# Optimization experiments

Hardware: AMD Instinct MI355X
Metric: run time of the kernel (lower is better)

## Reference

```python
import jax, jax.numpy as jnp
import numpy as np

L1_COST = 1000.0
ENTROPY_COST = 5e-05


def setup_inputs() -> dict:
    key = jax.random.key(0)
    k1, k2 = jax.random.split(key)
    inputs = jax.random.normal(k1, (8, 4096, 256), dtype=jnp.float32)
    # xavier_uniform for [K, D]: bound = sqrt(6/(K+D))
    K, D = 1024, 256
    bound = np.sqrt(6.0 / (K + D)).astype(np.float32)
    codebook = jax.random.uniform(k2, (K, D), dtype=jnp.float32, minval=-bound, maxval=bound)
    return {"inputs": inputs, "codebook": codebook}


def reference(inputs, codebook):
    D = codebook.shape[1]
    flat = inputs.reshape(-1, D)                                  # [N, D]
    norm_C = codebook / jnp.linalg.norm(codebook, axis=1, keepdims=True)   # [K, D]
    flat = flat / jnp.linalg.norm(flat, axis=1, keepdims=True)    # [N, D]
    distances = jax.nn.softmax(flat @ norm_C.T, axis=1)           # [N, K]
    reconstruction = (distances @ norm_C).reshape(inputs.shape)   # [B, S, D]
    # l1_loss(distances, zeros) == mean(|distances|)
    l1 = jnp.mean(jnp.abs(distances))
    # entropy term: mean_i sum_k [ -log_softmax(distances) @ distances.T ]_{ik}
    # = mean_i ( -log_softmax(distances)_i . colsum(distances) ), an O(N*K) equivalent
    log_sm = jax.nn.log_softmax(distances, axis=1)                # [N, K]
    col_sum = jnp.sum(distances, axis=0)                          # [K]
    entropy = jnp.mean(-(log_sm @ col_sum))
    loss = L1_COST * l1 + ENTROPY_COST * entropy
    return reconstruction, loss
```

## Files before the change

### kernel.cpp

```cpp
#include <hip/hip_runtime.h>
#include <cstdint>

#define N_ROWS 32768
#define KDIM 1024
#define DDIM 256

typedef __attribute__((ext_vector_type(8))) short bf16x8;
typedef __attribute__((ext_vector_type(4))) float f32x4;

__device__ __forceinline__ unsigned short f2bf(float f) {
  unsigned int u = __float_as_uint(f);
  u += 0x7FFFu + ((u >> 16) & 1u);
  return (unsigned short)(u >> 16);
}

__device__ __forceinline__ void gload_lds16(const void* g, void* l) {
  __builtin_amdgcn_global_load_lds(
      (const __attribute__((address_space(1))) unsigned int*)(uintptr_t)g,
      (__attribute__((address_space(3))) unsigned int*)(unsigned int)(uintptr_t)l,
      16, 0, 0);
}


__global__ __launch_bounds__(256) void k_norm_cb(const float* __restrict__ cb,
                                                 unsigned short* __restrict__ Cn,
                                                 unsigned short* __restrict__ CnT) {
  const int wid = threadIdx.x >> 6, lane = threadIdx.x & 63;
  const int k = blockIdx.x * 4 + wid;
  float4 v = ((const float4*)(cb + (size_t)k * DDIM))[lane];
  float s = v.x * v.x + v.y * v.y + v.z * v.z + v.w * v.w;
#pragma unroll
  for (int m = 32; m; m >>= 1) s += __shfl_xor(s, m, 64);
  const float rn = 1.0f / sqrtf(s);
  ushort4 p;
  p.x = f2bf(v.x * rn); p.y = f2bf(v.y * rn);
  p.z = f2bf(v.z * rn); p.w = f2bf(v.w * rn);
  const int kb = lane >> 3;
  const int physA = ((lane & 7) >> 1) ^ (k & 3);
  *(ushort4*)(Cn + (size_t)(k >> 6) * 16384 + kb * 2048 + (k & 63) * 32 + physA * 8 + (lane & 1) * 4) = p;
  const int sgl = k >> 5, c31 = k & 31, ch = c31 >> 3, cw = c31 & 7;
  const unsigned short pv[4] = {p.x, p.y, p.z, p.w};
#pragma unroll
  for (int j = 0; j < 4; ++j) {
    const int d = lane * 4 + j;
    CnT[(size_t)sgl * 8192 + d * 32 + ((ch ^ j) * 8) + cw] = pv[j];
  }
}

__global__ __launch_bounds__(512, 2) void k_all(const float* __restrict__ x,
                                                const unsigned short* __restrict__ Cn,
                                                const unsigned short* __restrict__ CnT,
                                                float* __restrict__ part,
                                                float* __restrict__ lse_part,
                                                float* __restrict__ out) {
  __shared__ unsigned short Cb[4][16384];
  __shared__ unsigned short Ps[128 * 72];
  __shared__ float csl[1024];
  __shared__ float rs[128], qs[128], irl[128];
  __shared__ float lse_sh[2];

  const int tid = threadIdx.x, wid = tid >> 6, lane = tid & 63;
  const int l15 = lane & 15, l4 = lane >> 4;
  const int wm = wid >> 1, wn = wid & 1;
  const int rb = blockIdx.x;
  if (tid < 128) { rs[tid] = 0.f; qs[tid] = 0.f; }
  for (int j = tid; j < 1024; j += 512) csl[j] = 0.f;

#pragma unroll
  for (int i = 0; i < 4; ++i) {
    const int off = i * 8192 + wid * 1024 + lane * 16;
    gload_lds16((const char*)Cn + off, (char*)Cb[2] + off);
    gload_lds16((const char*)Cn + 32768 + off, (char*)Cb[3] + off);
  }

  unsigned short* Xs = &Cb[0][0];
#pragma unroll
  for (int p16 = 0; p16 < 16; ++p16) {
    const int row = p16 * 8 + wid;
    float4 v = ((const float4*)(x + (size_t)(rb * 128 + row) * DDIM))[lane];
    float s = v.x * v.x + v.y * v.y + v.z * v.z + v.w * v.w;
#pragma unroll
    for (int m = 32; m; m >>= 1) s += __shfl_xor(s, m, 64);
    const float rn = 1.0f / sqrtf(s);
    ushort4 p;
    p.x = f2bf(v.x * rn); p.y = f2bf(v.y * rn);
    p.z = f2bf(v.z * rn); p.w = f2bf(v.w * rn);
    *(ushort4*)&Xs[(lane >> 3) * 4096 + row * 32 + (lane & 7) * 4] = p;
  }
  __syncthreads();
  bf16x8 areg[2][8];
#pragma unroll
  for (int mi = 0; mi < 2; ++mi)
#pragma unroll
    for (int kb = 0; kb < 8; ++kb)
      areg[mi][kb] = *(const bf16x8*)&Xs[kb * 4096 + (wm * 32 + mi * 16 + l15) * 32 + l4 * 8];

  const int xsw = l4 ^ (l15 & 3);

  float se[2][4], sq[2][4];
#pragma unroll
  for (int mi = 0; mi < 2; ++mi)
#pragma unroll
    for (int reg = 0; reg < 4; ++reg) { se[mi][reg] = 0.f; sq[mi][reg] = 0.f; }
  for (int kt = 0; kt < 16; ++kt) {
    __syncthreads();
    {
      const char* src = (kt <= 13) ? (const char*)Cn + (size_t)(kt + 2) * 32768
                      : (kt == 14) ? (const char*)Cn
                                   : (const char*)CnT;
      char* dst = (char*)Cb[kt & 3];
#pragma unroll
      for (int i = 0; i < 4; ++i) {
        const int off = i * 8192 + wid * 1024 + lane * 16;
        gload_lds16(src + off, dst + off);
      }
    }
    const unsigned short* B = Cb[(kt + 2) & 3];
    f32x4 acc[2][2] = {};
#pragma unroll
    for (int kb = 0; kb < 8; ++kb) {
      bf16x8 b[2];
#pragma unroll
      for (int ni = 0; ni < 2; ++ni)
        b[ni] = *(const bf16x8*)&B[kb * 2048 + (wn * 32 + ni * 16 + l15) * 32 + xsw * 8];
#pragma unroll
      for (int mi = 0; mi < 2; ++mi)
#pragma unroll
        for (int ni = 0; ni < 2; ++ni)
          acc[mi][ni] = __builtin_amdgcn_mfma_f32_16x16x32_bf16(areg[mi][kb], b[ni], acc[mi][ni], 0, 0, 0);
    }
#pragma unroll
    for (int mi = 0; mi < 2; ++mi)
#pragma unroll
      for (int reg = 0; reg < 4; ++reg)
#pragma unroll
        for (int ni = 0; ni < 2; ++ni) {
          const float e = __expf(acc[mi][ni][reg]);
          se[mi][reg] += e; sq[mi][reg] += e * e;
        }
  }
#pragma unroll
  for (int mi = 0; mi < 2; ++mi)
#pragma unroll
    for (int reg = 0; reg < 4; ++reg) {
#pragma unroll
      for (int m = 1; m < 16; m <<= 1) {
        se[mi][reg] += __shfl_xor(se[mi][reg], m, 64);
        sq[mi][reg] += __shfl_xor(sq[mi][reg], m, 64);
      }
    }
  if (l15 == 0) {
#pragma unroll
    for (int mi = 0; mi < 2; ++mi)
#pragma unroll
      for (int reg = 0; reg < 4; ++reg) {
        const int row = wm * 32 + mi * 16 + l4 * 4 + reg;
        atomicAdd(&rs[row], se[mi][reg]);
        atomicAdd(&qs[row], sq[mi][reg]);
      }
  }
  __syncthreads();
  if (tid < 128) {
    const float r = rs[tid];
    const float ir = 1.0f / r;
    irl[tid] = ir;
    float lse = logf((float)(KDIM + 1) + 0.5f * qs[tid] * ir * ir);
#pragma unroll
    for (int m = 32; m; m >>= 1) lse += __shfl_xor(lse, m, 64);
    if ((tid & 63) == 0) lse_sh[tid >> 6] = lse;
  }
  __syncthreads();
  float ir[2][4];
#pragma unroll
  for (int mi = 0; mi < 2; ++mi)
#pragma unroll
    for (int reg = 0; reg < 4; ++reg)
      ir[mi][reg] = irl[wm * 32 + mi * 16 + l4 * 4 + reg];

  f32x4 O[2][8] = {};
  const int psw_r = l15 >> 1;
  for (int kt = 0; kt < 16; ++kt) {
    const int cslot = (kt & 1) ? 0 : 2;
    const int tslot = cslot | 1;
    const int nslot = (kt & 1) ? 2 : 0;
    if (kt < 15) {
#pragma unroll
      for (int i = 0; i < 4; ++i) {
        const int off = i * 8192 + wid * 1024 + lane * 16;
        gload_lds16((const char*)Cn + (size_t)(kt + 1) * 32768 + off, (char*)Cb[nslot] + off);
      }
    }
    f32x4 S[2][2] = {};
#pragma unroll
    for (int kb = 0; kb < 8; ++kb) {
      bf16x8 b[2];
#pragma unroll
      for (int ni = 0; ni < 2; ++ni)
        b[ni] = *(const bf16x8*)&Cb[cslot][kb * 2048 + (wn * 32 + ni * 16 + l15) * 32 + xsw * 8];
#pragma unroll
      for (int mi = 0; mi < 2; ++mi)
#pragma unroll
        for (int ni = 0; ni < 2; ++ni)
          S[mi][ni] = __builtin_amdgcn_mfma_f32_16x16x32_bf16(areg[mi][kb], b[ni], S[mi][ni], 0, 0, 0);
    }
    float cs[2] = {0.f, 0.f};
#pragma unroll
    for (int mi = 0; mi < 2; ++mi)
#pragma unroll
      for (int reg = 0; reg < 4; ++reg) {
        const int row = wm * 32 + mi * 16 + l4 * 4 + reg;
        const int pswz = (l4 * 2 + (reg >> 1)) & 7;
#pragma unroll
        for (int ni = 0; ni < 2; ++ni) {
          const float e = __expf(S[mi][ni][reg]);
          const int chl = wn * 4 + ni * 2 + (l15 >> 3);
          Ps[row * 72 + ((chl ^ pswz) * 8) + (l15 & 7)] = f2bf(e);
          cs[ni] += e * ir[mi][reg];
        }
      }
#pragma unroll
    for (int ni = 0; ni < 2; ++ni) {
      float v = cs[ni];
      v += __shfl_xor(v, 16, 64);
      v += __shfl_xor(v, 32, 64);
      if (lane < 16) atomicAdd(&csl[kt * 64 + wn * 32 + ni * 16 + l15], v);
    }
    __syncthreads();
    if (kt < 15) {
#pragma unroll
      for (int i = 0; i < 4; ++i) {
        const int off = i * 8192 + wid * 1024 + lane * 16;
        gload_lds16((const char*)CnT + (size_t)(kt + 1) * 32768 + off, (char*)Cb[nslot + 1] + off);
      }
    }
#pragma unroll
    for (int kb2 = 0; kb2 < 2; ++kb2) {
      bf16x8 a2[2], b2[8];
#pragma unroll
      for (int mi = 0; mi < 2; ++mi) {
        const int row = wm * 32 + mi * 16 + l15;
        a2[mi] = *(const bf16x8*)&Ps[row * 72 + (((kb2 * 4 + l4) ^ psw_r) * 8)];
      }
#pragma unroll
      for (int ni = 0; ni < 8; ++ni) {
        const int d = wn * 128 + ni * 16 + l15;
        b2[ni] = *(const bf16x8*)&Cb[tslot][kb2 * 8192 + d * 32 + xsw * 8];
      }
#pragma unroll
      for (int mi = 0; mi < 2; ++mi)
#pragma unroll
        for (int ni = 0; ni < 8; ++ni)
          O[mi][ni] = __builtin_amdgcn_mfma_f32_16x16x32_bf16(a2[mi], b2[ni], O[mi][ni], 0, 0, 0);
    }
    __syncthreads();
  }

#pragma unroll
  for (int mi = 0; mi < 2; ++mi)
#pragma unroll
    for (int reg = 0; reg < 4; ++reg) {
      const int row = wm * 32 + mi * 16 + l4 * 4 + reg;
      const float irv = ir[mi][reg];
#pragma unroll
      for (int ni = 0; ni < 8; ++ni) {
        const int d = wn * 128 + ni * 16 + l15;
        out[(size_t)(rb * 128 + row) * DDIM + d] = O[mi][ni][reg] * irv;
      }
    }
  for (int j = tid; j < 1024; j += 512) part[rb * 1024 + j] = csl[j];
  if (tid == 0) lse_part[rb] = lse_sh[0] + lse_sh[1];
}

__global__ __launch_bounds__(256) void k_final(const float* __restrict__ part,
                                               const float* __restrict__ lse_part,
                                               float* __restrict__ acc3) {
  __shared__ float sh1[4], sh2[4], shl[4];
  const int tid = threadIdx.x, lane = tid & 63, w = tid >> 6;
  const int bh = tid & 15;
  const int kh = tid >> 4;
  const int k = blockIdx.x * 16 + kh;
  float s = 0.f;
#pragma unroll
  for (int m = 0; m < 16; ++m) s += part[(size_t)(bh * 16 + m) * 1024 + k];
#pragma unroll
  for (int m = 1; m < 16; m <<= 1) s += __shfl_xor(s, m, 64);
  float s1 = ((lane & 15) == 0) ? s : 0.f;
  float s2 = ((lane & 15) == 0) ? s * s : 0.f;
  s1 += __shfl_xor(s1, 16, 64); s2 += __shfl_xor(s2, 16, 64);
  s1 += __shfl_xor(s1, 32, 64); s2 += __shfl_xor(s2, 32, 64);
  if (lane == 0) { sh1[w] = s1; sh2[w] = s2; }
  float l = 0.f;
  if (blockIdx.x == 0) {
    l = lse_part[tid];
#pragma unroll
    for (int m = 1; m < 64; m <<= 1) l += __shfl_xor(l, m, 64);
  }
  if (lane == 0) shl[w] = l;
  __syncthreads();
  if (tid == 0) {
    atomicAdd(&acc3[0], sh1[0] + sh1[1] + sh1[2] + sh1[3]);
    atomicAdd(&acc3[1], sh2[0] + sh2[1] + sh2[2] + sh2[3]);
    if (blockIdx.x == 0) atomicAdd(&acc3[2], shl[0] + shl[1] + shl[2] + shl[3]);
  }
}

__global__ __launch_bounds__(64) void k_loss(const float* __restrict__ acc3,
                                             float* __restrict__ out) {
  if (threadIdx.x == 0) {
    const double S = acc3[0];
    const double Q = acc3[1];
    const double L = acc3[2];
    const double entropy = (S * L - Q) / (double)N_ROWS;
    const double l1 = S / ((double)N_ROWS * (double)KDIM);
    out[(size_t)N_ROWS * DDIM] = (float)(1000.0 * l1 + 5e-5 * entropy);
  }
}

extern "C" void kernel_launch(void* const* d_in, const int* in_sizes, int n_in,
                              void* d_out, int out_size, void* d_ws, size_t ws_size,
                              hipStream_t stream) {
  const float* x = (const float*)d_in[0];
  const float* cb = (const float*)d_in[1];
  float* out = (float*)d_out;
  char* ws = (char*)d_ws;

  unsigned short* Cn  = (unsigned short*)(ws + 0);
  unsigned short* CnT = (unsigned short*)(ws + 524288);
  float* part         = (float*)(ws + 1048576);
  float* lse_part     = (float*)(ws + 2097152);
  float* acc3         = (float*)(ws + 2098176);

  hipMemsetAsync(acc3, 0, 16, stream);
  k_norm_cb<<<256, 256, 0, stream>>>(cb, Cn, CnT);
  k_all<<<256, 512, 0, stream>>>(x, Cn, CnT, part, lse_part, out);
  k_final<<<64, 256, 0, stream>>>(part, lse_part, acc3);
  k_loss<<<1, 64, 0, stream>>>(acc3, out);
}
```

Baseline: 152.3 us.

## Halve row tile to 64, shrink LDS ring, use global atomics for reductions

The fused kernel now processes 64 rows per block instead of 128, across 512 blocks. It uses a smaller 64KB double-buffered LDS ring and splits the second pass into 32 half-width codebook tiles, which lets more blocks be resident per CU. Column sums and log-sum-exp partials are accumulated with global atomics, replacing the separate per-block partial buffers and the extra final reduction kernel. In exchange, each block re-streams the full codebook twice, so total codebook traffic doubles, and float atomic accumulation order becomes nondeterministic.

Result: slower. 174.6 us (+14.6%).

```diff
diff --git a/kernel.cpp b/kernel.cpp
--- a/kernel.cpp
+++ b/kernel.cpp
@@ -21,6 +21,23 @@
       16, 0, 0);
 }
 
+
+__device__ __forceinline__ void stage_cn32(const unsigned short* Cn, char* dstBase, int kt, int tid) {
+  const int t = kt >> 1, h = kt & 1;
+#pragma unroll
+  for (int i = 0; i < 2; ++i) {
+    const int o = i * 4096 + tid * 8;
+    const size_t g = (size_t)t * 16384 + (size_t)(o >> 10) * 2048 + (size_t)h * 1024 + (o & 1023);
+    gload_lds16((const char*)(Cn + g), dstBase + (size_t)o * 2);
+  }
+}
+__device__ __forceinline__ void stage_cnt32(const unsigned short* CnT, char* dstBase, int kt, int tid) {
+#pragma unroll
+  for (int i = 0; i < 2; ++i) {
+    const int o = i * 4096 + tid * 8;
+    gload_lds16((const char*)(CnT + (size_t)kt * 8192 + o), dstBase + (size_t)o * 2);
+  }
+}
 
 __global__ __launch_bounds__(256) void k_norm_cb(const float* __restrict__ cb,
                                                  unsigned short* __restrict__ Cn,
@@ -47,37 +64,35 @@
   }
 }
 
-__global__ __launch_bounds__(512, 2) void k_all(const float* __restrict__ x,
+__global__ __launch_bounds__(512, 4) void k_all(const float* __restrict__ x,
                                                 const unsigned short* __restrict__ Cn,
                                                 const unsigned short* __restrict__ CnT,
-                                                float* __restrict__ part,
-                                                float* __restrict__ lse_part,
+                                                float* __restrict__ colsum_g,
+                                                float* __restrict__ accL,
                                                 float* __restrict__ out) {
-  __shared__ unsigned short Cb[4][16384];
-  __shared__ unsigned short Ps[128 * 72];
+  __shared__ __align__(16) unsigned short Ring[32768];
+  __shared__ __align__(16) unsigned short Ps[64 * 40];
   __shared__ float csl[1024];
-  __shared__ float rs[128], qs[128], irl[128];
-  __shared__ float lse_sh[2];
+  __shared__ float rs[64], qs[64], irl[64];
 
   const int tid = threadIdx.x, wid = tid >> 6, lane = tid & 63;
   const int l15 = lane & 15, l4 = lane >> 4;
   const int wm = wid >> 1, wn = wid & 1;
   const int rb = blockIdx.x;
-  if (tid < 128) { rs[tid] = 0.f; qs[tid] = 0.f; }
+  if (tid < 64) { rs[tid] = 0.f; qs[tid] = 0.f; }
   for (int j = tid; j < 1024; j += 512) csl[j] = 0.f;
 
 #pragma unroll
   for (int i = 0; i < 4; ++i) {
-    const int off = i * 8192 + wid * 1024 + lane * 16;
-    gload_lds16((const char*)Cn + off, (char*)Cb[2] + off);
-    gload_lds16((const char*)Cn + 32768 + off, (char*)Cb[3] + off);
-  }
-
-  unsigned short* Xs = &Cb[0][0];
-#pragma unroll
-  for (int p16 = 0; p16 < 16; ++p16) {
-    const int row = p16 * 8 + wid;
-    float4 v = ((const float4*)(x + (size_t)(rb * 128 + row) * DDIM))[lane];
+    const int off = i * 8192 + tid * 16;
+    gload_lds16((const char*)Cn + off, (char*)Ring + off);
+  }
+
+  unsigned short* Xs = &Ring[16384];
+#pragma unroll
+  for (int p8 = 0; p8 < 8; ++p8) {
+    const int row = p8 * 8 + wid;
+    float4 v = ((const float4*)(x + (size_t)(rb * 64 + row) * DDIM))[lane];
     float s = v.x * v.x + v.y * v.y + v.z * v.z + v.w * v.w;
 #pragma unroll
     for (int m = 32; m; m >>= 1) s += __shfl_xor(s, m, 64);
@@ -85,231 +100,156 @@
     ushort4 p;
     p.x = f2bf(v.x * rn); p.y = f2bf(v.y * rn);
     p.z = f2bf(v.z * rn); p.w = f2bf(v.w * rn);
-    *(ushort4*)&Xs[(lane >> 3) * 4096 + row * 32 + (lane & 7) * 4] = p;
-  }
-  __syncthreads();
-  bf16x8 areg[2][8];
-#pragma unroll
-  for (int mi = 0; mi < 2; ++mi)
-#pragma unroll
-    for (int kb = 0; kb < 8; ++kb)
-      areg[mi][kb] = *(const bf16x8*)&Xs[kb * 4096 + (wm * 32 + mi * 16 + l15) * 32 + l4 * 8];
+    *(ushort4*)&Xs[(lane >> 3) * 2048 + row * 32 + (lane & 7) * 4] = p;
+  }
+  __syncthreads();
+  bf16x8 areg[8];
+#pragma unroll
+  for (int kb = 0; kb < 8; ++kb)
+    areg[kb] = *(const bf16x8*)&Xs[kb * 2048 + (wm * 16 + l15) * 32 + l4 * 8];
+  __syncthreads();
 
   const int xsw = l4 ^ (l15 & 3);
 
-  float se[2][4], sq[2][4];
-#pragma unroll
-  for (int mi = 0; mi < 2; ++mi)
-#pragma unroll
-    for (int reg = 0; reg < 4; ++reg) { se[mi][reg] = 0.f; sq[mi][reg] = 0.f; }
+  float se[4] = {0.f, 0.f, 0.f, 0.f}, sq[4] = {0.f, 0.f, 0.f, 0.f};
   for (int kt = 0; kt < 16; ++kt) {
-    __syncthreads();
-    {
-      const char* src = (kt <= 13) ? (const char*)Cn + (size_t)(kt + 2) * 32768
-                      : (kt == 14) ? (const char*)Cn
-                                   : (const char*)CnT;
-      char* dst = (char*)Cb[kt & 3];
+    if (kt < 15) {
+      const char* src = (const char*)Cn + (size_t)(kt + 1) * 32768;
+      char* dst = (char*)Ring + ((kt + 1) & 1) * 32768;
 #pragma unroll
       for (int i = 0; i < 4; ++i) {
-        const int off = i * 8192 + wid * 1024 + lane * 16;
+        const int off = i * 8192 + tid * 16;
         gload_lds16(src + off, dst + off);
       }
-    }
-    const unsigned short* B = Cb[(kt + 2) & 3];
-    f32x4 acc[2][2] = {};
+    } else {
+      stage_cn32(Cn, (char*)Ring, 0, tid);
+    }
+    const unsigned short* B = &Ring[(kt & 1) * 16384];
+    f32x4 acc[2] = {};
 #pragma unroll
     for (int kb = 0; kb < 8; ++kb) {
-      bf16x8 b[2];
-#pragma unroll
-      for (int ni = 0; ni < 2; ++ni)
-        b[ni] = *(const bf16x8*)&B[kb * 2048 + (wn * 32 + ni * 16 + l15) * 32 + xsw * 8];
-#pragma unroll
-      for (int mi = 0; mi < 2; ++mi)
-#pragma unroll
-        for (int ni = 0; ni < 2; ++ni)
-          acc[mi][ni] = __builtin_amdgcn_mfma_f32_16x16x32_bf16(areg[mi][kb], b[ni], acc[mi][ni], 0, 0, 0);
-    }
-#pragma unroll
-    for (int mi = 0; mi < 2; ++mi)
-#pragma unroll
-      for (int reg = 0; reg < 4; ++reg)
-#pragma unroll
-        for (int ni = 0; ni < 2; ++ni) {
-          const float e = __expf(acc[mi][ni][reg]);
-          se[mi][reg] += e; sq[mi][reg] += e * e;
-        }
-  }
-#pragma unroll
-  for (int mi = 0; mi < 2; ++mi)
+      bf16x8 b0 = *(const bf16x8*)&B[kb * 2048 + (wn * 32 + l15) * 32 + xsw * 8];
+      bf16x8 b1 = *(const bf16x8*)&B[kb * 2048 + (wn * 32 + 16 + l15) * 32 + xsw * 8];
+      acc[0] = __builtin_amdgcn_mfma_f32_16x16x32_bf16(areg[kb], b0, acc[0], 0, 0, 0);
+      acc[1] = __builtin_amdgcn_mfma_f32_16x16x32_bf16(areg[kb], b1, acc[1], 0, 0, 0);
+    }
+#pragma unroll
+    for (int reg = 0; reg < 4; ++reg)
+#pragma unroll
+      for (int ni = 0; ni < 2; ++ni) {
+        const float e = __expf(acc[ni][reg]);
+        se[reg] += e; sq[reg] += e * e;
+      }
+    __syncthreads();
+  }
+  stage_cnt32(CnT, (char*)Ring + 32768, 0, tid);
+
+#pragma unroll
+  for (int reg = 0; reg < 4; ++reg) {
+#pragma unroll
+    for (int m = 1; m < 16; m <<= 1) {
+      se[reg] += __shfl_xor(se[reg], m, 64);
+      sq[reg] += __shfl_xor(sq[reg], m, 64);
+    }
+  }
+  if (l15 == 0) {
 #pragma unroll
     for (int reg = 0; reg < 4; ++reg) {
-#pragma unroll
-      for (int m = 1; m < 16; m <<= 1) {
-        se[mi][reg] += __shfl_xor(se[mi][reg], m, 64);
-        sq[mi][reg] += __shfl_xor(sq[mi][reg], m, 64);
-      }
-    }
-  if (l15 == 0) {
-#pragma unroll
-    for (int mi = 0; mi < 2; ++mi)
-#pragma unroll
-      for (int reg = 0; reg < 4; ++reg) {
-        const int row = wm * 32 + mi * 16 + l4 * 4 + reg;
-        atomicAdd(&rs[row], se[mi][reg]);
-        atomicAdd(&qs[row], sq[mi][reg]);
-      }
-  }
-  __syncthreads();
-  if (tid < 128) {
+      const int row = wm * 16 + l4 * 4 + reg;
+      atomicAdd(&rs[row], se[reg]);
+      atomicAdd(&qs[row], sq[reg]);
+    }
+  }
+  __syncthreads();
+  if (tid < 64) {
     const float r = rs[tid];
-    const float ir = 1.0f / r;
-    irl[tid] = ir;
-    float lse = logf((float)(KDIM + 1) + 0.5f * qs[tid] * ir * ir);
+    const float irv = 1.0f / r;
+    irl[tid] = irv;
+    float lse = logf((float)(KDIM + 1) + 0.5f * qs[tid] * irv * irv);
 #pragma unroll
     for (int m = 32; m; m >>= 1) lse += __shfl_xor(lse, m, 64);
-    if ((tid & 63) == 0) lse_sh[tid >> 6] = lse;
-  }
-  __syncthreads();
-  float ir[2][4];
-#pragma unroll
-  for (int mi = 0; mi < 2; ++mi)
-#pragma unroll
-    for (int reg = 0; reg < 4; ++reg)
-      ir[mi][reg] = irl[wm * 32 + mi * 16 + l4 * 4 + reg];
-
-  f32x4 O[2][8] = {};
-  const int psw_r = l15 >> 1;
-  for (int kt = 0; kt < 16; ++kt) {
-    const int cslot = (kt & 1) ? 0 : 2;
-    const int tslot = cslot | 1;
-    const int nslot = (kt & 1) ? 2 : 0;
-    if (kt < 15) {
-#pragma unroll
-      for (int i = 0; i < 4; ++i) {
-        const int off = i * 8192 + wid * 1024 + lane * 16;
-        gload_lds16((const char*)Cn + (size_t)(kt + 1) * 32768 + off, (char*)Cb[nslot] + off);
-      }
-    }
-    f32x4 S[2][2] = {};
+    if (tid == 0) atomicAdd(accL, lse);
+  }
+  __syncthreads();
+  float irr[4];
+#pragma unroll
+  for (int reg = 0; reg < 4; ++reg) irr[reg] = irl[wm * 16 + l4 * 4 + reg];
+
+  f32x4 O[8] = {};
+  for (int kt = 0; kt < 32; ++kt) {
+    const int cur = kt & 1;
+    if (kt < 31) {
+      const int ns = (kt + 1) & 1;
+      stage_cn32(Cn, (char*)Ring + ns * 16384, kt + 1, tid);
+      stage_cnt32(CnT, (char*)Ring + 32768 + ns * 16384, kt + 1, tid);
+    }
+    const unsigned short* Bc = &Ring[cur * 8192];
+    f32x4 S = {};
 #pragma unroll
     for (int kb = 0; kb < 8; ++kb) {
-      bf16x8 b[2];
-#pragma unroll
-      for (int ni = 0; ni < 2; ++ni)
-        b[ni] = *(const bf16x8*)&Cb[cslot][kb * 2048 + (wn * 32 + ni * 16 + l15) * 32 + xsw * 8];
-#pragma unroll
-      for (int mi = 0; mi < 2; ++mi)
-#pragma unroll
-        for (int ni = 0; ni < 2; ++ni)
-          S[mi][ni] = __builtin_amdgcn_mfma_f32_16x16x32_bf16(areg[mi][kb], b[ni], S[mi][ni], 0, 0, 0);
-    }
-    float cs[2] = {0.f, 0.f};
-#pragma unroll
-    for (int mi = 0; mi < 2; ++mi)
-#pragma unroll
-      for (int reg = 0; reg < 4; ++reg) {
-        const int row = wm * 32 + mi * 16 + l4 * 4 + reg;
-        const int pswz = (l4 * 2 + (reg >> 1)) & 7;
-#pragma unroll
-        for (int ni = 0; ni < 2; ++ni) {
-          const float e = __expf(S[mi][ni][reg]);
-          const int chl = wn * 4 + ni * 2 + (l15 >> 3);
-          Ps[row * 72 + ((chl ^ pswz) * 8) + (l15 & 7)] = f2bf(e);
-          cs[ni] += e * ir[mi][reg];
-        }
-      }
-#pragma unroll
-    for (int ni = 0; ni < 2; ++ni) {
-      float v = cs[ni];
-      v += __shfl_xor(v, 16, 64);
-      v += __shfl_xor(v, 32, 64);
-      if (lane < 16) atomicAdd(&csl[kt * 64 + wn * 32 + ni * 16 + l15], v);
+      bf16x8 b = *(const bf16x8*)&Bc[kb * 1024 + (wn * 16 + l15) * 32 + xsw * 8];
+      S = __builtin_amdgcn_mfma_f32_16x16x32_bf16(areg[kb], b, S, 0, 0, 0);
+    }
+    float cs = 0.f;
+#pragma unroll
+    for (int reg = 0; reg < 4; ++reg) {
+      const float e = __expf(S[reg]);
+      const int row = wm * 16 + l4 * 4 + reg;
+      Ps[row * 40 + wn * 16 + l15] = f2bf(e);
+      cs += e * irr[reg];
+    }
+    cs += __shfl_xor(cs, 16, 64);
+    cs += __shfl_xor(cs, 32, 64);
+    if (lane < 16) atomicAdd(&csl[kt * 32 + wn * 16 + l15], cs);
+    asm volatile("s_waitcnt lgkmcnt(0)" ::: "memory");
+    __builtin_amdgcn_s_barrier();
+    __builtin_amdgcn_sched_barrier(0);
+    const unsigned short* Bt = &Ring[16384 + cur * 8192];
+    bf16x8 a2 = *(const bf16x8*)&Ps[(wm * 16 + l15) * 40 + l4 * 8];
+#pragma unroll
+    for (int ni = 0; ni < 8; ++ni) {
+      const int d = wn * 128 + ni * 16 + l15;
+      bf16x8 b2 = *(const bf16x8*)&Bt[d * 32 + ((l4 ^ (d & 3)) * 8)];
+      O[ni] = __builtin_amdgcn_mfma_f32_16x16x32_bf16(a2, b2, O[ni], 0, 0, 0);
     }
     __syncthreads();
-    if (kt < 15) {
-#pragma unroll
-      for (int i = 0; i < 4; ++i) {
-        const int off = i * 8192 + wid * 1024 + lane * 16;
-        gload_lds16((const char*)CnT + (size_t)(kt + 1) * 32768 + off, (char*)Cb[nslot + 1] + off);
-      }
-    }
-#pragma unroll
-    for (int kb2 = 0; kb2 < 2; ++kb2) {
-      bf16x8 a2[2], b2[8];
-#pragma unroll
-      for (int mi = 0; mi < 2; ++mi) {
-        const int row = wm * 32 + mi * 16 + l15;
-        a2[mi] = *(const bf16x8*)&Ps[row * 72 + (((kb2 * 4 + l4) ^ psw_r) * 8)];
-      }
-#pragma unroll
-      for (int ni = 0; ni < 8; ++ni) {
-        const int d = wn * 128 + ni * 16 + l15;
-        b2[ni] = *(const bf16x8*)&Cb[tslot][kb2 * 8192 + d * 32 + xsw * 8];
-      }
-#pragma unroll
-      for (int mi = 0; mi < 2; ++mi)
-#pragma unroll
-        for (int ni = 0; ni < 8; ++ni)
-          O[mi][ni] = __builtin_amdgcn_mfma_f32_16x16x32_bf16(a2[mi], b2[ni], O[mi][ni], 0, 0, 0);
-    }
-    __syncthreads();
-  }
-
-#pragma unroll
-  for (int mi = 0; mi < 2; ++mi)
-#pragma unroll
-    for (int reg = 0; reg < 4; ++reg) {
-      const int row = wm * 32 + mi * 16 + l4 * 4 + reg;
-      const float irv = ir[mi][reg];
-#pragma unroll
-      for (int ni = 0; ni < 8; ++ni) {
-        const int d = wn * 128 + ni * 16 + l15;
-        out[(size_t)(rb * 128 + row) * DDIM + d] = O[mi][ni][reg] * irv;
-      }
-    }
-  for (int j = tid; j < 1024; j += 512) part[rb * 1024 + j] = csl[j];
-  if (tid == 0) lse_part[rb] = lse_sh[0] + lse_sh[1];
-}
-
-__global__ __launch_bounds__(256) void k_final(const float* __restrict__ part,
-                                               const float* __restrict__ lse_part,
-                                               float* __restrict__ acc3) {
-  __shared__ float sh1[4], sh2[4], shl[4];
+  }
+
+#pragma unroll
+  for (int reg = 0; reg < 4; ++reg) {
+    const int row = wm * 16 + l4 * 4 + reg;
+    const float irv = irr[reg];
+#pragma unroll
+    for (int ni = 0; ni < 8; ++ni) {
+      const int d = wn * 128 + ni * 16 + l15;
+      out[(size_t)(rb * 64 + row) * DDIM + d] = O[ni][reg] * irv;
+    }
+  }
+  for (int j = tid; j < 1024; j += 512) atomicAdd(&colsum_g[j], csl[j]);
+}
+
+__global__ __launch_bounds__(256) void k_loss(const float* __restrict__ colsum_g,
+                                              const float* __restrict__ accL,
+                                              float* __restrict__ out) {
+  __shared__ float sh1[4], sh2[4];
   const int tid = threadIdx.x, lane = tid & 63, w = tid >> 6;
-  const int bh = tid & 15;
-  const int kh = tid >> 4;
-  const int k = blockIdx.x * 16 + kh;
-  float s = 0.f;
-#pragma unroll
-  for (int m = 0; m < 16; ++m) s += part[(size_t)(bh * 16 + m) * 1024 + k];
-#pragma unroll
-  for (int m = 1; m < 16; m <<= 1) s += __shfl_xor(s, m, 64);
-  float s1 = ((lane & 15) == 0) ? s : 0.f;
-  float s2 = ((lane & 15) == 0) ? s * s : 0.f;
-  s1 += __shfl_xor(s1, 16, 64); s2 += __shfl_xor(s2, 16, 64);
-  s1 += __shfl_xor(s1, 32, 64); s2 += __shfl_xor(s2, 32, 64);
-  if (lane == 0) { sh1[w] = s1; sh2[w] = s2; }
-  float l = 0.f;
-  if (blockIdx.x == 0) {
-    l = lse_part[tid];
-#pragma unroll
-    for (int m = 1; m < 64; m <<= 1) l += __shfl_xor(l, m, 64);
-  }
-  if (lane == 0) shl[w] = l;
+  float s = 0.f, q = 0.f;
+#pragma unroll
+  for (int j = 0; j < 4; ++j) {
+    const float c = colsum_g[tid + j * 256];
+    s += c; q += c * c;
+  }
+#pragma unroll
+  for (int m = 1; m < 64; m <<= 1) {
+    s += __shfl_xor(s, m, 64);
+    q += __shfl_xor(q, m, 64);
+  }
+  if (lane == 0) { sh1[w] = s; sh2[w] = q; }
   __syncthreads();
   if (tid == 0) {
-    atomicAdd(&acc3[0], sh1[0] + sh1[1] + sh1[2] + sh1[3]);
-    atomicAdd(&acc3[1], sh2[0] + sh2[1] + sh2[2] + sh2[3]);
-    if (blockIdx.x == 0) atomicAdd(&acc3[2], shl[0] + shl[1] + shl[2] + shl[3]);
-  }
-}
-
-__global__ __launch_bounds__(64) void k_loss(const float* __restrict__ acc3,
-                                             float* __restrict__ out) {
-  if (threadIdx.x == 0) {
-    const double S = acc3[0];
-    const double Q = acc3[1];
-    const double L = acc3[2];
+    const double S = (double)sh1[0] + sh1[1] + sh1[2] + sh1[3];
+    const double Q = (double)sh2[0] + sh2[1] + sh2[2] + sh2[3];
+    const double L = accL[0];
     const double entropy = (S * L - Q) / (double)N_ROWS;
     const double l1 = S / ((double)N_ROWS * (double)KDIM);
     out[(size_t)N_ROWS * DDIM] = (float)(1000.0 * l1 + 5e-5 * entropy);
@@ -326,13 +266,11 @@
 
   unsigned short* Cn  = (unsigned short*)(ws + 0);
   unsigned short* CnT = (unsigned short*)(ws + 524288);
-  float* part         = (float*)(ws + 1048576);
-  float* lse_part     = (float*)(ws + 2097152);
-  float* acc3         = (float*)(ws + 2098176);
-
-  hipMemsetAsync(acc3, 0, 16, stream);
+  float* colsum_g     = (float*)(ws + 1048576);
+  float* accL         = (float*)(ws + 1052672);
+
+  hipMemsetAsync(ws + 1048576, 0, 4100, stream);
   k_norm_cb<<<256, 256, 0, stream>>>(cb, Cn, CnT);
-  k_all<<<256, 512, 0, stream>>>(x, Cn, CnT, part, lse_part, out);
-  k_final<<<64, 256, 0, stream>>>(part, lse_part, acc3);
-  k_loss<<<1, 64, 0, stream>>>(acc3, out);
-}
+  k_all<<<512, 512, 0, stream>>>(x, Cn, CnT, colsum_g, accL, out);
+  k_loss<<<1, 256, 0, stream>>>(colsum_g, accL, out);
+}
```

## Fuse codebook normalization, main pass and loss reduction into one persistent kernel

Applied to the files above, without the earlier changes.

Merges the codebook-normalize kernel, main kernel, final reduction and loss kernels into a single launch. A grid-wide atomic counter barrier waits until all blocks have written the normalized codebook, and a last-block-done counter performs the final loss reduction from atomically accumulated column sums. It also replaces several __syncthreads with explicit vmcnt waits plus s_barrier so codebook tile prefetches overlap compute. This removes three launch gaps and the intermediate partial-sum round trip, but relies on all 256 blocks being co-resident for the spin barrier and adds global atomics.

Result: slower. 218.8 us (+43.6%).

```diff
diff --git a/kernel.cpp b/kernel.cpp
--- a/kernel.cpp
+++ b/kernel.cpp
@@ -22,42 +22,22 @@
 }
 
 
-__global__ __launch_bounds__(256) void k_norm_cb(const float* __restrict__ cb,
-                                                 unsigned short* __restrict__ Cn,
-                                                 unsigned short* __restrict__ CnT) {
-  const int wid = threadIdx.x >> 6, lane = threadIdx.x & 63;
-  const int k = blockIdx.x * 4 + wid;
-  float4 v = ((const float4*)(cb + (size_t)k * DDIM))[lane];
-  float s = v.x * v.x + v.y * v.y + v.z * v.z + v.w * v.w;
-#pragma unroll
-  for (int m = 32; m; m >>= 1) s += __shfl_xor(s, m, 64);
-  const float rn = 1.0f / sqrtf(s);
-  ushort4 p;
-  p.x = f2bf(v.x * rn); p.y = f2bf(v.y * rn);
-  p.z = f2bf(v.z * rn); p.w = f2bf(v.w * rn);
-  const int kb = lane >> 3;
-  const int physA = ((lane & 7) >> 1) ^ (k & 3);
-  *(ushort4*)(Cn + (size_t)(k >> 6) * 16384 + kb * 2048 + (k & 63) * 32 + physA * 8 + (lane & 1) * 4) = p;
-  const int sgl = k >> 5, c31 = k & 31, ch = c31 >> 3, cw = c31 & 7;
-  const unsigned short pv[4] = {p.x, p.y, p.z, p.w};
-#pragma unroll
-  for (int j = 0; j < 4; ++j) {
-    const int d = lane * 4 + j;
-    CnT[(size_t)sgl * 8192 + d * 32 + ((ch ^ j) * 8) + cw] = pv[j];
-  }
-}
-
-__global__ __launch_bounds__(512, 2) void k_all(const float* __restrict__ x,
-                                                const unsigned short* __restrict__ Cn,
-                                                const unsigned short* __restrict__ CnT,
-                                                float* __restrict__ part,
-                                                float* __restrict__ lse_part,
-                                                float* __restrict__ out) {
+__global__ __launch_bounds__(512, 2) void k_fused(const float* __restrict__ x,
+                                                  const float* __restrict__ cb,
+                                                  unsigned short* __restrict__ Cn,
+                                                  unsigned short* __restrict__ CnT,
+                                                  float* __restrict__ colsum_g,
+                                                  float* __restrict__ accL,
+                                                  int* __restrict__ cnt1,
+                                                  int* __restrict__ cnt2,
+                                                  float* __restrict__ out) {
   __shared__ unsigned short Cb[4][16384];
   __shared__ unsigned short Ps[128 * 72];
   __shared__ float csl[1024];
   __shared__ float rs[128], qs[128], irl[128];
   __shared__ float lse_sh[2];
+  __shared__ float sh1[4], sh2[4];
+  __shared__ int lastf;
 
   const int tid = threadIdx.x, wid = tid >> 6, lane = tid & 63;
   const int l15 = lane & 15, l4 = lane >> 4;
@@ -66,11 +46,26 @@
   if (tid < 128) { rs[tid] = 0.f; qs[tid] = 0.f; }
   for (int j = tid; j < 1024; j += 512) csl[j] = 0.f;
 
-#pragma unroll
-  for (int i = 0; i < 4; ++i) {
-    const int off = i * 8192 + wid * 1024 + lane * 16;
-    gload_lds16((const char*)Cn + off, (char*)Cb[2] + off);
-    gload_lds16((const char*)Cn + 32768 + off, (char*)Cb[3] + off);
+  if (wid < 4) {
+    const int k = rb * 4 + wid;
+    float4 v = ((const float4*)(cb + (size_t)k * DDIM))[lane];
+    float s = v.x * v.x + v.y * v.y + v.z * v.z + v.w * v.w;
+#pragma unroll
+    for (int m = 32; m; m >>= 1) s += __shfl_xor(s, m, 64);
+    const float rn = 1.0f / sqrtf(s);
+    ushort4 p;
+    p.x = f2bf(v.x * rn); p.y = f2bf(v.y * rn);
+    p.z = f2bf(v.z * rn); p.w = f2bf(v.w * rn);
+    const int kb = lane >> 3;
+    const int physA = ((lane & 7) >> 1) ^ (k & 3);
+    *(ushort4*)(Cn + (size_t)(k >> 6) * 16384 + kb * 2048 + (k & 63) * 32 + physA * 8 + (lane & 1) * 4) = p;
+    const int sgl = k >> 5, c31 = k & 31, ch = c31 >> 3, cw = c31 & 7;
+    const unsigned short pv[4] = {p.x, p.y, p.z, p.w};
+#pragma unroll
+    for (int j = 0; j < 4; ++j) {
+      const int d = lane * 4 + j;
+      CnT[(size_t)sgl * 8192 + d * 32 + ((ch ^ j) * 8) + cw] = pv[j];
+    }
   }
 
   unsigned short* Xs = &Cb[0][0];
@@ -87,13 +82,35 @@
     p.z = f2bf(v.z * rn); p.w = f2bf(v.w * rn);
     *(ushort4*)&Xs[(lane >> 3) * 4096 + row * 32 + (lane & 7) * 4] = p;
   }
-  __syncthreads();
+
+  __syncthreads();
+  __threadfence();
+  if (tid == 0) {
+    __hip_atomic_fetch_add(cnt1, 1, __ATOMIC_RELEASE, __HIP_MEMORY_SCOPE_AGENT);
+    while (__hip_atomic_load(cnt1, __ATOMIC_ACQUIRE, __HIP_MEMORY_SCOPE_AGENT) < 256)
+      __builtin_amdgcn_s_sleep(2);
+  }
+  __syncthreads();
+
+#pragma unroll
+  for (int i = 0; i < 4; ++i) {
+    const int off = i * 8192 + wid * 1024 + lane * 16;
+    gload_lds16((const char*)Cn + off, (char*)Cb[2] + off);
+  }
+#pragma unroll
+  for (int i = 0; i < 4; ++i) {
+    const int off = i * 8192 + wid * 1024 + lane * 16;
+    gload_lds16((const char*)Cn + 32768 + off, (char*)Cb[3] + off);
+  }
+
   bf16x8 areg[2][8];
 #pragma unroll
   for (int mi = 0; mi < 2; ++mi)
 #pragma unroll
     for (int kb = 0; kb < 8; ++kb)
       areg[mi][kb] = *(const bf16x8*)&Xs[kb * 4096 + (wm * 32 + mi * 16 + l15) * 32 + l4 * 8];
+  asm volatile("s_waitcnt lgkmcnt(0)" ::: "memory");
+  __builtin_amdgcn_s_barrier();
 
   const int xsw = l4 ^ (l15 & 3);
 
@@ -103,7 +120,6 @@
 #pragma unroll
     for (int reg = 0; reg < 4; ++reg) { se[mi][reg] = 0.f; sq[mi][reg] = 0.f; }
   for (int kt = 0; kt < 16; ++kt) {
-    __syncthreads();
     {
       const char* src = (kt <= 13) ? (const char*)Cn + (size_t)(kt + 2) * 32768
                       : (kt == 14) ? (const char*)Cn
@@ -115,6 +131,8 @@
         gload_lds16(src + off, dst + off);
       }
     }
+    asm volatile("s_waitcnt vmcnt(8)" ::: "memory");
+    __builtin_amdgcn_s_barrier();
     const unsigned short* B = Cb[(kt + 2) & 3];
     f32x4 acc[2][2] = {};
 #pragma unroll
@@ -162,14 +180,15 @@
   __syncthreads();
   if (tid < 128) {
     const float r = rs[tid];
-    const float ir = 1.0f / r;
-    irl[tid] = ir;
-    float lse = logf((float)(KDIM + 1) + 0.5f * qs[tid] * ir * ir);
+    const float irv = 1.0f / r;
+    irl[tid] = irv;
+    float lse = logf((float)(KDIM + 1) + 0.5f * qs[tid] * irv * irv);
 #pragma unroll
     for (int m = 32; m; m >>= 1) lse += __shfl_xor(lse, m, 64);
     if ((tid & 63) == 0) lse_sh[tid >> 6] = lse;
   }
   __syncthreads();
+  if (tid == 0) atomicAdd(accL, lse_sh[0] + lse_sh[1]);
   float ir[2][4];
 #pragma unroll
   for (int mi = 0; mi < 2; ++mi)
@@ -183,12 +202,11 @@
     const int cslot = (kt & 1) ? 0 : 2;
     const int tslot = cslot | 1;
     const int nslot = (kt & 1) ? 2 : 0;
-    if (kt < 15) {
-#pragma unroll
-      for (int i = 0; i < 4; ++i) {
-        const int off = i * 8192 + wid * 1024 + lane * 16;
-        gload_lds16((const char*)Cn + (size_t)(kt + 1) * 32768 + off, (char*)Cb[nslot] + off);
-      }
+    const int nt = (kt < 15) ? kt + 1 : 15;
+#pragma unroll
+    for (int i = 0; i < 4; ++i) {
+      const int off = i * 8192 + wid * 1024 + lane * 16;
+      gload_lds16((const char*)Cn + (size_t)nt * 32768 + off, (char*)Cb[nslot] + off);
     }
     f32x4 S[2][2] = {};
 #pragma unroll
@@ -225,13 +243,13 @@
       v += __shfl_xor(v, 32, 64);
       if (lane < 16) atomicAdd(&csl[kt * 64 + wn * 32 + ni * 16 + l15], v);
     }
-    __syncthreads();
-    if (kt < 15) {
-#pragma unroll
-      for (int i = 0; i < 4; ++i) {
-        const int off = i * 8192 + wid * 1024 + lane * 16;
-        gload_lds16((const char*)CnT + (size_t)(kt + 1) * 32768 + off, (char*)Cb[nslot + 1] + off);
-      }
+    asm volatile("s_waitcnt vmcnt(4) lgkmcnt(0)" ::: "memory");
+    __builtin_amdgcn_s_barrier();
+    __builtin_amdgcn_sched_barrier(0);
+#pragma unroll
+    for (int i = 0; i < 4; ++i) {
+      const int off = i * 8192 + wid * 1024 + lane * 16;
+      gload_lds16((const char*)CnT + (size_t)nt * 32768 + off, (char*)Cb[nslot + 1] + off);
     }
 #pragma unroll
     for (int kb2 = 0; kb2 < 2; ++kb2) {
@@ -252,8 +270,10 @@
         for (int ni = 0; ni < 8; ++ni)
           O[mi][ni] = __builtin_amdgcn_mfma_f32_16x16x32_bf16(a2[mi], b2[ni], O[mi][ni], 0, 0, 0);
     }
-    __syncthreads();
-  }
+    asm volatile("s_waitcnt vmcnt(4)" ::: "memory");
+    __builtin_amdgcn_s_barrier();
+  }
+  __syncthreads();
 
 #pragma unroll
   for (int mi = 0; mi < 2; ++mi)
@@ -267,52 +287,38 @@
         out[(size_t)(rb * 128 + row) * DDIM + d] = O[mi][ni][reg] * irv;
       }
     }
-  for (int j = tid; j < 1024; j += 512) part[rb * 1024 + j] = csl[j];
-  if (tid == 0) lse_part[rb] = lse_sh[0] + lse_sh[1];
-}
-
-__global__ __launch_bounds__(256) void k_final(const float* __restrict__ part,
-                                               const float* __restrict__ lse_part,
-                                               float* __restrict__ acc3) {
-  __shared__ float sh1[4], sh2[4], shl[4];
-  const int tid = threadIdx.x, lane = tid & 63, w = tid >> 6;
-  const int bh = tid & 15;
-  const int kh = tid >> 4;
-  const int k = blockIdx.x * 16 + kh;
-  float s = 0.f;
-#pragma unroll
-  for (int m = 0; m < 16; ++m) s += part[(size_t)(bh * 16 + m) * 1024 + k];
-#pragma unroll
-  for (int m = 1; m < 16; m <<= 1) s += __shfl_xor(s, m, 64);
-  float s1 = ((lane & 15) == 0) ? s : 0.f;
-  float s2 = ((lane & 15) == 0) ? s * s : 0.f;
-  s1 += __shfl_xor(s1, 16, 64); s2 += __shfl_xor(s2, 16, 64);
-  s1 += __shfl_xor(s1, 32, 64); s2 += __shfl_xor(s2, 32, 64);
-  if (lane == 0) { sh1[w] = s1; sh2[w] = s2; }
-  float l = 0.f;
-  if (blockIdx.x == 0) {
-    l = lse_part[tid];
-#pragma unroll
-    for (int m = 1; m < 64; m <<= 1) l += __shfl_xor(l, m, 64);
-  }
-  if (lane == 0) shl[w] = l;
-  __syncthreads();
+  for (int j = tid; j < 1024; j += 512) atomicAdd(&colsum_g[j], csl[j]);
+
   if (tid == 0) {
-    atomicAdd(&acc3[0], sh1[0] + sh1[1] + sh1[2] + sh1[3]);
-    atomicAdd(&acc3[1], sh2[0] + sh2[1] + sh2[2] + sh2[3]);
-    if (blockIdx.x == 0) atomicAdd(&acc3[2], shl[0] + shl[1] + shl[2] + shl[3]);
-  }
-}
-
-__global__ __launch_bounds__(64) void k_loss(const float* __restrict__ acc3,
-                                             float* __restrict__ out) {
-  if (threadIdx.x == 0) {
-    const double S = acc3[0];
-    const double Q = acc3[1];
-    const double L = acc3[2];
-    const double entropy = (S * L - Q) / (double)N_ROWS;
-    const double l1 = S / ((double)N_ROWS * (double)KDIM);
-    out[(size_t)N_ROWS * DDIM] = (float)(1000.0 * l1 + 5e-5 * entropy);
+    __threadfence();
+    const int old = __hip_atomic_fetch_add(cnt2, 1, __ATOMIC_ACQ_REL, __HIP_MEMORY_SCOPE_AGENT);
+    lastf = (old == 255);
+  }
+  __syncthreads();
+  if (lastf) {
+    if (tid < 256) {
+      float s = 0.f, q = 0.f;
+#pragma unroll
+      for (int j = 0; j < 4; ++j) {
+        const float c = __hip_atomic_load(&colsum_g[tid + j * 256], __ATOMIC_RELAXED, __HIP_MEMORY_SCOPE_AGENT);
+        s += c; q += c * c;
+      }
+#pragma unroll
+      for (int m = 1; m < 64; m <<= 1) {
+        s += __shfl_xor(s, m, 64);
+        q += __shfl_xor(q, m, 64);
+      }
+      if (lane == 0) { sh1[tid >> 6] = s; sh2[tid >> 6] = q; }
+    }
+    __syncthreads();
+    if (tid == 0) {
+      const double S = (double)sh1[0] + sh1[1] + sh1[2] + sh1[3];
+      const double Q = (double)sh2[0] + sh2[1] + sh2[2] + sh2[3];
+      const double L = __hip_atomic_load(accL, __ATOMIC_RELAXED, __HIP_MEMORY_SCOPE_AGENT);
+      const double entropy = (S * L - Q) / (double)N_ROWS;
+      const double l1 = S / ((double)N_ROWS * (double)KDIM);
+      out[(size_t)N_ROWS * DDIM] = (float)(1000.0 * l1 + 5e-5 * entropy);
+    }
   }
 }
 
@@ -326,13 +332,11 @@
 
   unsigned short* Cn  = (unsigned short*)(ws + 0);
   unsigned short* CnT = (unsigned short*)(ws + 524288);
-  float* part         = (float*)(ws + 1048576);
-  float* lse_part     = (float*)(ws + 2097152);
-  float* acc3         = (float*)(ws + 2098176);
-
-  hipMemsetAsync(acc3, 0, 16, stream);
-  k_norm_cb<<<256, 256, 0, stream>>>(cb, Cn, CnT);
-  k_all<<<256, 512, 0, stream>>>(x, Cn, CnT, part, lse_part, out);
-  k_final<<<64, 256, 0, stream>>>(part, lse_part, acc3);
-  k_loss<<<1, 64, 0, stream>>>(acc3, out);
+  float* colsum_g     = (float*)(ws + 1048576);
+  float* accL         = (float*)(ws + 1052672);
+  int* cnt1           = (int*)(ws + 1052676);
+  int* cnt2           = (int*)(ws + 1052680);
+
+  hipMemsetAsync(ws + 1048576, 0, 4112, stream);
+  k_fused<<<256, 512, 0, stream>>>(x, cb, Cn, CnT, colsum_g, accL, cnt1, cnt2, out);
 }
```
